# Optimization experiments

Measured on AMD Instinct MI355X. Metric: run time of the kernel, lower is better.

The kernel has to match this reference:

```python
import jax, jax.numpy as jnp
import numpy as np

D = 256       # d_model
H = 8         # nhead
W = 2048      # num windows (single drop level)
T = 64        # max_tokens per window (drop_info['num_sampled_tokens'][dl])
FILL = 48
N = W * FILL  # total voxels


def setup_inputs() -> dict:
    key = jax.random.key(0)
    k0, k1, k2, k3 = jax.random.split(key, 4)
    voxel_feat = jax.random.normal(k0, (N, D), jnp.float32)
    pos_embed = jax.random.normal(k1, (N, D), jnp.float32)
    # nn.MultiheadAttention params: packed in_proj [3D, D] and out_proj [D, D]
    in_proj_w = jax.random.normal(k2, (3 * D, D), jnp.float32) * (1.0 / np.sqrt(D))
    in_proj_b = jnp.zeros((3 * D,), jnp.float32)
    out_proj_w = jax.random.normal(k3, (D, D), jnp.float32) * (1.0 / np.sqrt(D))
    out_proj_b = jnp.zeros((D,), jnp.float32)
    # each voxel assigned a (window, in-window-slot) pair; slots unique per window
    window_idx = (jnp.arange(N) // FILL).astype(jnp.int32)
    slot_idx = (jnp.arange(N) % FILL).astype(jnp.int32)
    return {
        'voxel_feat': voxel_feat, 'pos_embed': pos_embed,
        'in_proj_w': in_proj_w, 'in_proj_b': in_proj_b,
        'out_proj_w': out_proj_w, 'out_proj_b': out_proj_b,
        'window_idx': window_idx, 'slot_idx': slot_idx,
        'num_windows': W, 'max_tokens': T,
    }


def reference(voxel_feat, pos_embed, in_proj_w, in_proj_b, out_proj_w, out_proj_b,
              window_idx, slot_idx, num_windows, max_tokens):
    Dm = voxel_feat.shape[-1]
    hd = Dm // H  # head dim
    P = num_windows * max_tokens  # padded token count
    valid = window_idx.astype(jnp.int32) * max_tokens + slot_idx.astype(jnp.int32)

    # scatter voxels into padded dense windows
    feat = jnp.zeros((P, Dm), voxel_feat.dtype).at[valid].set(voxel_feat)
    pos = jnp.ones((P, Dm), voxel_feat.dtype).at[valid].set(pos_embed)
    kmask = jnp.zeros((P,), bool).at[valid].set(True).reshape(num_windows, max_tokens)  # True = valid key
    feat = feat.reshape(num_windows, max_tokens, Dm)
    pos = pos.reshape(num_windows, max_tokens, Dm)

    # MHA: q = k = feat + pos, v = feat (torch nn.MultiheadAttention math)
    Wq, Wk, Wv = jnp.split(in_proj_w, 3, axis=0)
    bq, bk, bv = jnp.split(in_proj_b, 3, axis=0)
    qk_in = feat + pos
    q = (qk_in @ Wq.T + bq).reshape(num_windows, max_tokens, H, hd)
    k = (qk_in @ Wk.T + bk).reshape(num_windows, max_tokens, H, hd)
    v = (feat @ Wv.T + bv).reshape(num_windows, max_tokens, H, hd)

    scale = 1.0 / np.sqrt(hd)
    scores = jnp.einsum('wqhd,wkhd->whqk', q, k) * scale  # [W, H, T, T]
    scores = jnp.where(kmask[:, None, None, :], scores, -jnp.inf)  # key_padding_mask
    attn = jax.nn.softmax(scores, axis=-1)
    out = jnp.einsum('whqk,wkhd->wqhd', attn, v).reshape(P, Dm)
    out = out @ out_proj_w.T + out_proj_b

    # gather valid tokens back to per-voxel output (padded rows dropped, as in original)
    return out[valid]
```

## Files before the change

kernel.cpp:

```cpp
#include <hip/hip_runtime.h>

#define DD   256
#define HH   8
#define HDIM 32
#define TT   64
#define WW   2048

typedef unsigned short u16;
typedef __attribute__((ext_vector_type(8))) __bf16 bf8_t;
typedef __attribute__((ext_vector_type(4))) float  f32x4;

__device__ __forceinline__ u16 f2bf(float x) {
  union { float f; unsigned u; } c; c.f = x;
  unsigned r = c.u + 0x7FFFu + ((c.u >> 16) & 1u);
  return (u16)(r >> 16);
}
__device__ __forceinline__ int pack2(float a, float b) {
  return (int)((unsigned)f2bf(a) | ((unsigned)f2bf(b) << 16));
}

__global__ void prep_weights(const float* __restrict__ inw, const float* __restrict__ outw,
                             u16* __restrict__ wq, u16* __restrict__ wo) {
  int i = blockIdx.x * blockDim.x + threadIdx.x;
  if (i < 768 * 256) wq[i] = f2bf(inw[i]);
  if (i < 256 * 256) wo[i] = f2bf(outw[i]);
}

__global__ void build_slots(const int* __restrict__ widx, const int* __restrict__ sidx,
                            int* __restrict__ wslots, int n) {
  int i = blockIdx.x * blockDim.x + threadIdx.x;
  if (i < n) wslots[widx[i] * TT + sidx[i]] = i;
}

__global__ __launch_bounds__(512) void fused_attn(
    const float* __restrict__ feat, const float* __restrict__ pos,
    const u16* __restrict__ wqkv,
    const u16* __restrict__ wout,
    const float* __restrict__ inb, const float* __restrict__ outb,
    const int* __restrict__ wslots, float* __restrict__ out) {

  __shared__ int tl[TT];
  __shared__ u16 xqk[TT][72];
  __shared__ u16 xvs[TT][72];
  __shared__ u16 qld[TT][264];
  __shared__ u16 kld[TT][264];
  __shared__ u16 vtl[DD][72];

  const int t    = threadIdx.x;
  const int h    = t >> 6;
  const int lane = t & 63;
  const int g    = lane >> 4;
  const int l16  = lane & 15;
  const int w    = blockIdx.x;

  if (t < TT) tl[t] = wslots[w * TT + t];
  __syncthreads();

  const f32x4 zf = {0.f, 0.f, 0.f, 0.f};

  f32x4 qa[4][2], ka[4][2], va[2][4];
#pragma unroll
  for (int mt = 0; mt < 4; ++mt)
#pragma unroll
    for (int nt = 0; nt < 2; ++nt) { qa[mt][nt] = zf; ka[mt][nt] = zf; }
#pragma unroll
  for (int md = 0; md < 2; ++md)
#pragma unroll
    for (int nt = 0; nt < 4; ++nt) va[md][nt] = zf;

  const int stok = t >> 3;
  const int sds  = (t & 7) << 3;
  const int srow = tl[stok];

  for (int kc = 0; kc < 4; ++kc) {
    {
      union { u16 u[8]; bf8_t v; } aq, av_;
      if (srow >= 0) {
        const float4* fp = (const float4*)(feat + (size_t)srow * DD + kc * 64 + sds);
        const float4* pp = (const float4*)(pos  + (size_t)srow * DD + kc * 64 + sds);
        float4 f0 = fp[0], f1 = fp[1], p0 = pp[0], p1 = pp[1];
        float fr[8] = {f0.x, f0.y, f0.z, f0.w, f1.x, f1.y, f1.z, f1.w};
        float pr[8] = {p0.x, p0.y, p0.z, p0.w, p1.x, p1.y, p1.z, p1.w};
#pragma unroll
        for (int j = 0; j < 8; ++j) { aq.u[j] = f2bf(fr[j] + pr[j]); av_.u[j] = f2bf(fr[j]); }
      } else {
#pragma unroll
        for (int j = 0; j < 8; ++j) { aq.u[j] = 0; av_.u[j] = 0; }
      }
      *(bf8_t*)&xqk[stok][sds] = aq.v;
      *(bf8_t*)&xvs[stok][sds] = av_.v;
    }
    __syncthreads();

    bf8_t ax[4][2], bx[4][2];
#pragma unroll
    for (int mt = 0; mt < 4; ++mt)
#pragma unroll
      for (int ks = 0; ks < 2; ++ks) {
        ax[mt][ks] = *(const bf8_t*)&xqk[mt * 16 + l16][ks * 32 + g * 8];
        bx[mt][ks] = *(const bf8_t*)&xvs[mt * 16 + l16][ks * 32 + g * 8];
      }

#pragma unroll
    for (int ks = 0; ks < 2; ++ks) {
      const int kb = kc * 64 + ks * 32 + g * 8;
#pragma unroll
      for (int nt = 0; nt < 2; ++nt) {
        bf8_t bwq = *(const bf8_t*)(wqkv + (size_t)(h * 32 + nt * 16 + l16) * DD + kb);
#pragma unroll
        for (int mt = 0; mt < 4; ++mt)
          qa[mt][nt] = __builtin_amdgcn_mfma_f32_16x16x32_bf16(ax[mt][ks], bwq, qa[mt][nt], 0, 0, 0);
        bf8_t bwk = *(const bf8_t*)(wqkv + (size_t)(256 + h * 32 + nt * 16 + l16) * DD + kb);
#pragma unroll
        for (int mt = 0; mt < 4; ++mt)
          ka[mt][nt] = __builtin_amdgcn_mfma_f32_16x16x32_bf16(ax[mt][ks], bwk, ka[mt][nt], 0, 0, 0);
      }
#pragma unroll
      for (int md = 0; md < 2; ++md) {
        bf8_t awv = *(const bf8_t*)(wqkv + (size_t)(512 + h * 32 + md * 16 + l16) * DD + kb);
#pragma unroll
        for (int nt = 0; nt < 4; ++nt)
          va[md][nt] = __builtin_amdgcn_mfma_f32_16x16x32_bf16(awv, bx[nt][ks], va[md][nt], 0, 0, 0);
      }
    }
    __syncthreads();
  }

#pragma unroll
  for (int nt = 0; nt < 2; ++nt) {
    float bq = inb[h * 32 + nt * 16 + l16];
    float bk = inb[256 + h * 32 + nt * 16 + l16];
#pragma unroll
    for (int mt = 0; mt < 4; ++mt)
#pragma unroll
      for (int r = 0; r < 4; ++r) {
        qld[mt * 16 + 4 * g + r][h * 32 + nt * 16 + l16] = f2bf(qa[mt][nt][r] + bq);
        kld[mt * 16 + 4 * g + r][h * 32 + nt * 16 + l16] = f2bf(ka[mt][nt][r] + bk);
      }
  }
#pragma unroll
  for (int md = 0; md < 2; ++md)
#pragma unroll
    for (int r = 0; r < 4; ++r) {
      float bv = inb[512 + h * 32 + md * 16 + 4 * g + r];
#pragma unroll
      for (int nt = 0; nt < 4; ++nt)
        vtl[h * 32 + md * 16 + 4 * g + r][nt * 16 + l16] = f2bf(va[md][nt][r] + bv);
    }

  bf8_t akf[4], bqf[4];
#pragma unroll
  for (int mt = 0; mt < 4; ++mt) akf[mt] = *(const bf8_t*)&kld[mt * 16 + l16][h * 32 + g * 8];
#pragma unroll
  for (int nt = 0; nt < 4; ++nt) bqf[nt] = *(const bf8_t*)&qld[nt * 16 + l16][h * 32 + g * 8];

  f32x4 sa[4][4];
#pragma unroll
  for (int mt = 0; mt < 4; ++mt)
#pragma unroll
    for (int nt = 0; nt < 4; ++nt)
      sa[mt][nt] = __builtin_amdgcn_mfma_f32_16x16x32_bf16(akf[mt], bqf[nt], zf, 0, 0, 0);

  __syncthreads();

  bool vm[4][4];
#pragma unroll
  for (int mt = 0; mt < 4; ++mt)
#pragma unroll
    for (int r = 0; r < 4; ++r) vm[mt][r] = (tl[mt * 16 + 4 * g + r] >= 0);

  const float scale = 0.17677669529663687f;
  int pk[4][4][2];
#pragma unroll
  for (int nt = 0; nt < 4; ++nt) {
    float sv[4][4];
    float m = -3e38f;
#pragma unroll
    for (int mt = 0; mt < 4; ++mt)
#pragma unroll
      for (int r = 0; r < 4; ++r) {
        float s = vm[mt][r] ? sa[mt][nt][r] * scale : -3e38f;
        sv[mt][r] = s;
        m = fmaxf(m, s);
      }
    m = fmaxf(m, __shfl_xor(m, 16, 64));
    m = fmaxf(m, __shfl_xor(m, 32, 64));
    float sum = 0.f;
#pragma unroll
    for (int mt = 0; mt < 4; ++mt)
#pragma unroll
      for (int r = 0; r < 4; ++r) {
        float p = vm[mt][r] ? __expf(sv[mt][r] - m) : 0.f;
        sv[mt][r] = p;
        sum += p;
      }
    sum += __shfl_xor(sum, 16, 64);
    sum += __shfl_xor(sum, 32, 64);
    float inv = sum > 0.f ? 1.f / sum : 0.f;
#pragma unroll
    for (int mt = 0; mt < 4; ++mt)
#pragma unroll
      for (int rp = 0; rp < 2; ++rp)
        pk[mt][nt][rp] = pack2(sv[mt][2 * rp] * inv, sv[mt][2 * rp + 1] * inv);
  }

  bf8_t avf[2][2];
#pragma unroll
  for (int md = 0; md < 2; ++md)
#pragma unroll
    for (int kk = 0; kk < 2; ++kk)
      avf[md][kk] = *(const bf8_t*)&vtl[h * 32 + md * 16 + l16][kk * 32 + g * 8];

  f32x4 oa[2][4];
#pragma unroll
  for (int md = 0; md < 2; ++md)
#pragma unroll
    for (int nt = 0; nt < 4; ++nt) oa[md][nt] = zf;

#pragma unroll
  for (int kk = 0; kk < 2; ++kk) {
#pragma unroll
    for (int nt = 0; nt < 4; ++nt) {
      union { int wd[4]; bf8_t v; } bu;
#pragma unroll
      for (int wd = 0; wd < 4; ++wd) {
        int src = l16 + 16 * (2 * (g & 1) + (wd >> 1));
        int lo = __shfl(pk[2 * kk + 0][nt][wd & 1], src, 64);
        int hi = __shfl(pk[2 * kk + 1][nt][wd & 1], src, 64);
        bu.wd[wd] = (g & 2) ? hi : lo;
      }
#pragma unroll
      for (int md = 0; md < 2; ++md)
        oa[md][nt] = __builtin_amdgcn_mfma_f32_16x16x32_bf16(avf[md][kk], bu.v, oa[md][nt], 0, 0, 0);
    }
  }

#pragma unroll
  for (int md = 0; md < 2; ++md)
#pragma unroll
    for (int nt = 0; nt < 4; ++nt)
#pragma unroll
      for (int r = 0; r < 4; ++r)
        qld[nt * 16 + l16][h * 32 + md * 16 + 4 * g + r] = f2bf(oa[md][nt][r]);
  __syncthreads();

  f32x4 fa[4][2];
#pragma unroll
  for (int mt = 0; mt < 4; ++mt)
#pragma unroll
    for (int nt = 0; nt < 2; ++nt) fa[mt][nt] = zf;

#pragma unroll
  for (int kk = 0; kk < 8; ++kk) {
    bf8_t aa[4];
#pragma unroll
    for (int mt = 0; mt < 4; ++mt)
      aa[mt] = *(const bf8_t*)&qld[mt * 16 + l16][kk * 32 + g * 8];
#pragma unroll
    for (int nt = 0; nt < 2; ++nt) {
      bf8_t bw = *(const bf8_t*)(wout + (size_t)(h * 32 + nt * 16 + l16) * DD + kk * 32 + g * 8);
#pragma unroll
      for (int mt = 0; mt < 4; ++mt)
        fa[mt][nt] = __builtin_amdgcn_mfma_f32_16x16x32_bf16(aa[mt], bw, fa[mt][nt], 0, 0, 0);
    }
  }

#pragma unroll
  for (int nt = 0; nt < 2; ++nt) {
    float ob = outb[h * 32 + nt * 16 + l16];
#pragma unroll
    for (int mt = 0; mt < 4; ++mt)
#pragma unroll
      for (int r = 0; r < 4; ++r) {
        int tok = mt * 16 + 4 * g + r;
        int row = tl[tok];
        if (row >= 0)
          out[(size_t)row * DD + h * 32 + nt * 16 + l16] = fa[mt][nt][r] + ob;
      }
  }
}

extern "C" void kernel_launch(void* const* d_in, const int* in_sizes, int n_in,
                              void* d_out, int out_size, void* d_ws, size_t ws_size,
                              hipStream_t stream) {
  (void)n_in; (void)out_size; (void)ws_size;
  const float* feat = (const float*)d_in[0];
  const float* pos  = (const float*)d_in[1];
  const float* inw  = (const float*)d_in[2];
  const float* inb  = (const float*)d_in[3];
  const float* outw = (const float*)d_in[4];
  const float* outb = (const float*)d_in[5];
  const int*   widx = (const int*)d_in[6];
  const int*   sidx = (const int*)d_in[7];
  const int N = in_sizes[0] / DD;

  char* ws = (char*)d_ws;
  u16* wqkv   = (u16*)ws;
  u16* wout   = (u16*)(ws + 393216);
  int* wslots = (int*)(ws + 393216 + 131072);

  hipMemsetAsync(wslots, 0xFF, WW * TT * sizeof(int), stream);
  prep_weights<<<768, 256, 0, stream>>>(inw, outw, wqkv, wout);
  build_slots<<<(N + 255) / 256, 256, 0, stream>>>(widx, sidx, wslots, N);
  fused_attn<<<WW, 512, 0, stream>>>(feat, pos, wqkv, wout, inb, outb, wslots, (float*)d_out);
}
```

Before: 250.7 us.

## Alias shared buffers and split V and QK projections to cut LDS use

Shared memory is collapsed from five arrays into two aliased buffers. The whole feature row is now staged once, and the V projection runs before pos is added in place, followed by the Q/K projection. The aim is lower LDS use per block so more blocks fit per CU, plus fewer syncs inside the k-loop. The cost is extra barriers and an extra bf16 round-trip: q/k input becomes bf16(bf16(feat)+pos), which changes rounding slightly. The output store is also packed into an int2 write.

```diff
diff --git a/kernel.cpp b/kernel.cpp
--- a/kernel.cpp
+++ b/kernel.cpp
@@ -2,7 +2,6 @@
 
 #define DD   256
 #define HH   8
-#define HDIM 32
 #define TT   64
 #define WW   2048
 
@@ -14,6 +13,9 @@
   union { float f; unsigned u; } c; c.f = x;
   unsigned r = c.u + 0x7FFFu + ((c.u >> 16) & 1u);
   return (u16)(r >> 16);
+}
+__device__ __forceinline__ float bf2f(u16 x) {
+  union { unsigned u; float f; } c; c.u = ((unsigned)x) << 16; return c.f;
 }
 __device__ __forceinline__ int pack2(float a, float b) {
   return (int)((unsigned)f2bf(a) | ((unsigned)f2bf(b) << 16));
@@ -40,11 +42,8 @@
     const int* __restrict__ wslots, float* __restrict__ out) {
 
   __shared__ int tl[TT];
-  __shared__ u16 xqk[TT][72];
-  __shared__ u16 xvs[TT][72];
-  __shared__ u16 qld[TT][264];
-  __shared__ u16 kld[TT][264];
-  __shared__ u16 vtl[DD][72];
+  __shared__ u16 bufX[TT * 264];
+  __shared__ u16 bufY[DD * 72];
 
   const int t    = threadIdx.x;
   const int h    = t >> 6;
@@ -57,50 +56,89 @@
   __syncthreads();
 
   const f32x4 zf = {0.f, 0.f, 0.f, 0.f};
-
-  f32x4 qa[4][2], ka[4][2], va[2][4];
+  const int stok = t >> 3;
+  const int seg  = t & 7;
+  const int srow = tl[stok];
+
+  if (srow >= 0) {
+    const float4* fp = (const float4*)(feat + (size_t)srow * DD + seg * 32);
+    float4 f[8];
+#pragma unroll
+    for (int j = 0; j < 8; ++j) f[j] = fp[j];
+#pragma unroll
+    for (int c = 0; c < 4; ++c) {
+      union { u16 u[8]; bf8_t v; } r;
+#pragma unroll
+      for (int j = 0; j < 8; ++j) r.u[j] = f2bf(((const float*)f)[c * 8 + j]);
+      *(bf8_t*)&bufX[stok * 264 + seg * 32 + c * 8] = r.v;
+    }
+  } else {
+    union { u16 u[8]; bf8_t v; } z;
+#pragma unroll
+    for (int j = 0; j < 8; ++j) z.u[j] = 0;
+#pragma unroll
+    for (int c = 0; c < 4; ++c)
+      *(bf8_t*)&bufX[stok * 264 + seg * 32 + c * 8] = z.v;
+  }
+  __syncthreads();
+
+  f32x4 va[2][4];
+#pragma unroll
+  for (int md = 0; md < 2; ++md)
+#pragma unroll
+    for (int nt = 0; nt < 4; ++nt) va[md][nt] = zf;
+
+  for (int kc = 0; kc < 4; ++kc) {
+    bf8_t bx[4][2];
+#pragma unroll
+    for (int nt = 0; nt < 4; ++nt)
+#pragma unroll
+      for (int ks = 0; ks < 2; ++ks)
+        bx[nt][ks] = *(const bf8_t*)&bufX[(nt * 16 + l16) * 264 + kc * 64 + ks * 32 + g * 8];
+#pragma unroll
+    for (int ks = 0; ks < 2; ++ks) {
+      const int kb = kc * 64 + ks * 32 + g * 8;
+#pragma unroll
+      for (int md = 0; md < 2; ++md) {
+        bf8_t awv = *(const bf8_t*)(wqkv + (size_t)(512 + h * 32 + md * 16 + l16) * DD + kb);
+#pragma unroll
+        for (int nt = 0; nt < 4; ++nt)
+          va[md][nt] = __builtin_amdgcn_mfma_f32_16x16x32_bf16(awv, bx[nt][ks], va[md][nt], 0, 0, 0);
+      }
+    }
+  }
+  __syncthreads();
+
+  if (srow >= 0) {
+    const float4* pp = (const float4*)(pos + (size_t)srow * DD + seg * 32);
+    float4 p[8];
+#pragma unroll
+    for (int j = 0; j < 8; ++j) p[j] = pp[j];
+#pragma unroll
+    for (int c = 0; c < 4; ++c) {
+      union { u16 u[8]; bf8_t v; } xb, r;
+      xb.v = *(const bf8_t*)&bufX[stok * 264 + seg * 32 + c * 8];
+#pragma unroll
+      for (int j = 0; j < 8; ++j)
+        r.u[j] = f2bf(bf2f(xb.u[j]) + ((const float*)p)[c * 8 + j]);
+      *(bf8_t*)&bufX[stok * 264 + seg * 32 + c * 8] = r.v;
+    }
+  }
+  __syncthreads();
+
+  f32x4 qa[4][2], ka[4][2];
 #pragma unroll
   for (int mt = 0; mt < 4; ++mt)
 #pragma unroll
     for (int nt = 0; nt < 2; ++nt) { qa[mt][nt] = zf; ka[mt][nt] = zf; }
-#pragma unroll
-  for (int md = 0; md < 2; ++md)
-#pragma unroll
-    for (int nt = 0; nt < 4; ++nt) va[md][nt] = zf;
-
-  const int stok = t >> 3;
-  const int sds  = (t & 7) << 3;
-  const int srow = tl[stok];
 
   for (int kc = 0; kc < 4; ++kc) {
-    {
-      union { u16 u[8]; bf8_t v; } aq, av_;
-      if (srow >= 0) {
-        const float4* fp = (const float4*)(feat + (size_t)srow * DD + kc * 64 + sds);
-        const float4* pp = (const float4*)(pos  + (size_t)srow * DD + kc * 64 + sds);
-        float4 f0 = fp[0], f1 = fp[1], p0 = pp[0], p1 = pp[1];
-        float fr[8] = {f0.x, f0.y, f0.z, f0.w, f1.x, f1.y, f1.z, f1.w};
-        float pr[8] = {p0.x, p0.y, p0.z, p0.w, p1.x, p1.y, p1.z, p1.w};
-#pragma unroll
-        for (int j = 0; j < 8; ++j) { aq.u[j] = f2bf(fr[j] + pr[j]); av_.u[j] = f2bf(fr[j]); }
-      } else {
-#pragma unroll
-        for (int j = 0; j < 8; ++j) { aq.u[j] = 0; av_.u[j] = 0; }
-      }
-      *(bf8_t*)&xqk[stok][sds] = aq.v;
-      *(bf8_t*)&xvs[stok][sds] = av_.v;
-    }
-    __syncthreads();
-
-    bf8_t ax[4][2], bx[4][2];
-#pragma unroll
-    for (int mt = 0; mt < 4; ++mt)
-#pragma unroll
-      for (int ks = 0; ks < 2; ++ks) {
-        ax[mt][ks] = *(const bf8_t*)&xqk[mt * 16 + l16][ks * 32 + g * 8];
-        bx[mt][ks] = *(const bf8_t*)&xvs[mt * 16 + l16][ks * 32 + g * 8];
-      }
-
+    bf8_t ax[4][2];
+#pragma unroll
+    for (int mt = 0; mt < 4; ++mt)
+#pragma unroll
+      for (int ks = 0; ks < 2; ++ks)
+        ax[mt][ks] = *(const bf8_t*)&bufX[(mt * 16 + l16) * 264 + kc * 64 + ks * 32 + g * 8];
 #pragma unroll
     for (int ks = 0; ks < 2; ++ks) {
       const int kb = kc * 64 + ks * 32 + g * 8;
@@ -115,16 +153,9 @@
         for (int mt = 0; mt < 4; ++mt)
           ka[mt][nt] = __builtin_amdgcn_mfma_f32_16x16x32_bf16(ax[mt][ks], bwk, ka[mt][nt], 0, 0, 0);
       }
-#pragma unroll
-      for (int md = 0; md < 2; ++md) {
-        bf8_t awv = *(const bf8_t*)(wqkv + (size_t)(512 + h * 32 + md * 16 + l16) * DD + kb);
-#pragma unroll
-        for (int nt = 0; nt < 4; ++nt)
-          va[md][nt] = __builtin_amdgcn_mfma_f32_16x16x32_bf16(awv, bx[nt][ks], va[md][nt], 0, 0, 0);
-      }
-    }
-    __syncthreads();
-  }
+    }
+  }
+  __syncthreads();
 
 #pragma unroll
   for (int nt = 0; nt < 2; ++nt) {
@@ -134,10 +165,27 @@
     for (int mt = 0; mt < 4; ++mt)
 #pragma unroll
       for (int r = 0; r < 4; ++r) {
-        qld[mt * 16 + 4 * g + r][h * 32 + nt * 16 + l16] = f2bf(qa[mt][nt][r] + bq);
-        kld[mt * 16 + 4 * g + r][h * 32 + nt * 16 + l16] = f2bf(ka[mt][nt][r] + bk);
-      }
-  }
+        bufX[(mt * 16 + 4 * g + r) * 264 + h * 32 + nt * 16 + l16] = f2bf(qa[mt][nt][r] + bq);
+        bufY[(mt * 16 + 4 * g + r) * 264 + h * 32 + nt * 16 + l16] = f2bf(ka[mt][nt][r] + bk);
+      }
+  }
+  __syncthreads();
+
+  bf8_t akf[4], bqf[4];
+#pragma unroll
+  for (int mt = 0; mt < 4; ++mt) akf[mt] = *(const bf8_t*)&bufY[(mt * 16 + l16) * 264 + h * 32 + g * 8];
+#pragma unroll
+  for (int nt = 0; nt < 4; ++nt) bqf[nt] = *(const bf8_t*)&bufX[(nt * 16 + l16) * 264 + h * 32 + g * 8];
+
+  f32x4 sa[4][4];
+#pragma unroll
+  for (int mt = 0; mt < 4; ++mt)
+#pragma unroll
+    for (int nt = 0; nt < 4; ++nt)
+      sa[mt][nt] = __builtin_amdgcn_mfma_f32_16x16x32_bf16(akf[mt], bqf[nt], zf, 0, 0, 0);
+
+  __syncthreads();
+
 #pragma unroll
   for (int md = 0; md < 2; ++md)
 #pragma unroll
@@ -145,23 +193,8 @@
       float bv = inb[512 + h * 32 + md * 16 + 4 * g + r];
 #pragma unroll
       for (int nt = 0; nt < 4; ++nt)
-        vtl[h * 32 + md * 16 + 4 * g + r][nt * 16 + l16] = f2bf(va[md][nt][r] + bv);
-    }
-
-  bf8_t akf[4], bqf[4];
-#pragma unroll
-  for (int mt = 0; mt < 4; ++mt) akf[mt] = *(const bf8_t*)&kld[mt * 16 + l16][h * 32 + g * 8];
-#pragma unroll
-  for (int nt = 0; nt < 4; ++nt) bqf[nt] = *(const bf8_t*)&qld[nt * 16 + l16][h * 32 + g * 8];
-
-  f32x4 sa[4][4];
-#pragma unroll
-  for (int mt = 0; mt < 4; ++mt)
-#pragma unroll
-    for (int nt = 0; nt < 4; ++nt)
-      sa[mt][nt] = __builtin_amdgcn_mfma_f32_16x16x32_bf16(akf[mt], bqf[nt], zf, 0, 0, 0);
-
-  __syncthreads();
+        bufY[(h * 32 + md * 16 + 4 * g + r) * 72 + nt * 16 + l16] = f2bf(va[md][nt][r] + bv);
+    }
 
   bool vm[4][4];
 #pragma unroll
@@ -209,7 +242,7 @@
   for (int md = 0; md < 2; ++md)
 #pragma unroll
     for (int kk = 0; kk < 2; ++kk)
-      avf[md][kk] = *(const bf8_t*)&vtl[h * 32 + md * 16 + l16][kk * 32 + g * 8];
+      avf[md][kk] = *(const bf8_t*)&bufY[(h * 32 + md * 16 + l16) * 72 + kk * 32 + g * 8];
 
   f32x4 oa[2][4];
 #pragma unroll
@@ -238,10 +271,12 @@
 #pragma unroll
   for (int md = 0; md < 2; ++md)
 #pragma unroll
-    for (int nt = 0; nt < 4; ++nt)
-#pragma unroll
-      for (int r = 0; r < 4; ++r)
-        qld[nt * 16 + l16][h * 32 + md * 16 + 4 * g + r] = f2bf(oa[md][nt][r]);
+    for (int nt = 0; nt < 4; ++nt) {
+      union { int wd[2]; } pw;
+      pw.wd[0] = pack2(oa[md][nt][0], oa[md][nt][1]);
+      pw.wd[1] = pack2(oa[md][nt][2], oa[md][nt][3]);
+      *(int2*)&bufX[(nt * 16 + l16) * 264 + h * 32 + md * 16 + 4 * g] = make_int2(pw.wd[0], pw.wd[1]);
+    }
   __syncthreads();
 
   f32x4 fa[4][2];
@@ -255,7 +290,7 @@
     bf8_t aa[4];
 #pragma unroll
     for (int mt = 0; mt < 4; ++mt)
-      aa[mt] = *(const bf8_t*)&qld[mt * 16 + l16][kk * 32 + g * 8];
+      aa[mt] = *(const bf8_t*)&bufX[(mt * 16 + l16) * 264 + kk * 32 + g * 8];
 #pragma unroll
     for (int nt = 0; nt < 2; ++nt) {
       bf8_t bw = *(const bf8_t*)(wout + (size_t)(h * 32 + nt * 16 + l16) * DD + kk * 32 + g * 8);
```

New measurement: 255.7 us. 1.02x slower.

## Split fused window attention into a dense QKV GEMM kernel and an attention/out-proj kernel

Applied to the files above, without the earlier changes.

Replaces the single per-window fused kernel with two kernels. The first projects Q, K and V with a dense GEMM over the voxels, so padded tokens are not computed, and writes Q/K in bf16 plus V transposed per window. The second computes attention and the output projection with 256-thread blocks, two heads per wave, and a swizzled LDS layout. The aim is to cut wasted MFMA work on padding and to improve occupancy, at the cost of extra global round-trips for the Q/K/V intermediates and a scattered transposed V write. It also assumes N is a multiple of 64 and that unused V slots are never read unmasked (they can be uninitialized).

```diff
diff --git a/kernel.cpp b/kernel.cpp
--- a/kernel.cpp
+++ b/kernel.cpp
@@ -1,14 +1,14 @@
 #include <hip/hip_runtime.h>
 
-#define DD   256
-#define HH   8
-#define HDIM 32
-#define TT   64
-#define WW   2048
+#define DD 256
+#define TT 64
+#define WW 2048
 
 typedef unsigned short u16;
 typedef __attribute__((ext_vector_type(8))) __bf16 bf8_t;
 typedef __attribute__((ext_vector_type(4))) float  f32x4;
+
+#define XSW(tok, col) ((tok) * 256 + ((col) ^ (((tok) & 7) << 3)))
 
 __device__ __forceinline__ u16 f2bf(float x) {
   union { float f; unsigned u; } c; c.f = x;
@@ -32,22 +32,144 @@
   if (i < n) wslots[widx[i] * TT + sidx[i]] = i;
 }
 
-__global__ __launch_bounds__(512) void fused_attn(
+__global__ __launch_bounds__(256, 4) void qkv_gemm(
     const float* __restrict__ feat, const float* __restrict__ pos,
-    const u16* __restrict__ wqkv,
-    const u16* __restrict__ wout,
-    const float* __restrict__ inb, const float* __restrict__ outb,
+    const u16* __restrict__ wqkv, const float* __restrict__ inb,
+    const int* __restrict__ widx, const int* __restrict__ sidx,
+    u16* __restrict__ qc, u16* __restrict__ kc, u16* __restrict__ vt) {
+
+  __shared__ u16 xb[TT * 72];
+  __shared__ u16 cb[TT * 264];
+
+  const int t    = threadIdx.x;
+  const int wv   = t >> 6;
+  const int lane = t & 63;
+  const int g    = lane >> 4;
+  const int l16  = lane & 15;
+  const int m0   = blockIdx.x * 64;
+  const int p    = blockIdx.y;
+
+  const int svox = t >> 2;
+  const int sseg = t & 3;
+
+  const f32x4 zf = {0.f, 0.f, 0.f, 0.f};
+  f32x4 acc[4][4];
+#pragma unroll
+  for (int mt = 0; mt < 4; ++mt)
+#pragma unroll
+    for (int nt = 0; nt < 4; ++nt) acc[mt][nt] = zf;
+
+  for (int kc_ = 0; kc_ < 4; ++kc_) {
+    {
+      const float4* fp = (const float4*)(feat + (size_t)(m0 + svox) * DD + kc_ * 64 + sseg * 16);
+      float4 f[4];
+#pragma unroll
+      for (int j = 0; j < 4; ++j) f[j] = fp[j];
+      float fr[16];
+#pragma unroll
+      for (int j = 0; j < 16; ++j) fr[j] = ((const float*)f)[j];
+      if (p < 2) {
+        const float4* pp = (const float4*)(pos + (size_t)(m0 + svox) * DD + kc_ * 64 + sseg * 16);
+        float4 q[4];
+#pragma unroll
+        for (int j = 0; j < 4; ++j) q[j] = pp[j];
+#pragma unroll
+        for (int j = 0; j < 16; ++j) fr[j] += ((const float*)q)[j];
+      }
+#pragma unroll
+      for (int c = 0; c < 2; ++c) {
+        union { u16 u[8]; bf8_t v; } r;
+#pragma unroll
+        for (int j = 0; j < 8; ++j) r.u[j] = f2bf(fr[c * 8 + j]);
+        *(bf8_t*)&xb[svox * 72 + sseg * 16 + c * 8] = r.v;
+      }
+    }
+    __syncthreads();
+
+    if (p < 2) {
+      bf8_t ax[4][2];
+#pragma unroll
+      for (int mt = 0; mt < 4; ++mt)
+#pragma unroll
+        for (int ks = 0; ks < 2; ++ks)
+          ax[mt][ks] = *(const bf8_t*)&xb[(mt * 16 + l16) * 72 + ks * 32 + g * 8];
+#pragma unroll
+      for (int ks = 0; ks < 2; ++ks) {
+        const int kb = kc_ * 64 + ks * 32 + g * 8;
+#pragma unroll
+        for (int nt = 0; nt < 4; ++nt) {
+          bf8_t bw = *(const bf8_t*)(wqkv + (size_t)(p * 256 + wv * 64 + nt * 16 + l16) * DD + kb);
+#pragma unroll
+          for (int mt = 0; mt < 4; ++mt)
+            acc[mt][nt] = __builtin_amdgcn_mfma_f32_16x16x32_bf16(ax[mt][ks], bw, acc[mt][nt], 0, 0, 0);
+        }
+      }
+    } else {
+      bf8_t bx[4][2];
+#pragma unroll
+      for (int nt = 0; nt < 4; ++nt)
+#pragma unroll
+        for (int ks = 0; ks < 2; ++ks)
+          bx[nt][ks] = *(const bf8_t*)&xb[(nt * 16 + l16) * 72 + ks * 32 + g * 8];
+#pragma unroll
+      for (int ks = 0; ks < 2; ++ks) {
+        const int kb = kc_ * 64 + ks * 32 + g * 8;
+#pragma unroll
+        for (int mt = 0; mt < 4; ++mt) {
+          bf8_t aw = *(const bf8_t*)(wqkv + (size_t)(512 + wv * 64 + mt * 16 + l16) * DD + kb);
+#pragma unroll
+          for (int nt = 0; nt < 4; ++nt)
+            acc[mt][nt] = __builtin_amdgcn_mfma_f32_16x16x32_bf16(aw, bx[nt][ks], acc[mt][nt], 0, 0, 0);
+        }
+      }
+    }
+    __syncthreads();
+  }
+
+  if (p < 2) {
+#pragma unroll
+    for (int nt = 0; nt < 4; ++nt) {
+      float b = inb[p * 256 + wv * 64 + nt * 16 + l16];
+#pragma unroll
+      for (int mt = 0; mt < 4; ++mt)
+#pragma unroll
+        for (int r = 0; r < 4; ++r)
+          cb[(mt * 16 + 4 * g + r) * 264 + wv * 64 + nt * 16 + l16] = f2bf(acc[mt][nt][r] + b);
+    }
+    __syncthreads();
+    u16* dst = p ? kc : qc;
+#pragma unroll
+    for (int it = 0; it < 8; ++it) {
+      int i = it * 256 + t;
+      int row = i >> 5, c8 = (i & 31) * 8;
+      *(bf8_t*)&dst[(size_t)(m0 + row) * DD + c8] = *(const bf8_t*)&cb[row * 264 + c8];
+    }
+  } else {
+#pragma unroll
+    for (int nt = 0; nt < 4; ++nt) {
+      int vx = m0 + nt * 16 + l16;
+      size_t bw_ = (size_t)widx[vx] * (DD * TT) + sidx[vx];
+#pragma unroll
+      for (int mt = 0; mt < 4; ++mt)
+#pragma unroll
+        for (int r = 0; r < 4; ++r) {
+          int vd = wv * 64 + mt * 16 + 4 * g + r;
+          vt[bw_ + (size_t)vd * TT] = f2bf(acc[mt][nt][r] + inb[512 + vd]);
+        }
+    }
+  }
+}
+
+__global__ __launch_bounds__(256, 4) void attn_out(
+    const u16* __restrict__ qc, const u16* __restrict__ kc, const u16* __restrict__ vt,
+    const u16* __restrict__ wout, const float* __restrict__ outb,
     const int* __restrict__ wslots, float* __restrict__ out) {
 
   __shared__ int tl[TT];
-  __shared__ u16 xqk[TT][72];
-  __shared__ u16 xvs[TT][72];
-  __shared__ u16 qld[TT][264];
-  __shared__ u16 kld[TT][264];
-  __shared__ u16 vtl[DD][72];
+  __shared__ u16 ab[TT * 256];
 
   const int t    = threadIdx.x;
-  const int h    = t >> 6;
+  const int wv   = t >> 6;
   const int lane = t & 63;
   const int g    = lane >> 4;
   const int l16  = lane & 15;
@@ -58,207 +180,128 @@
 
   const f32x4 zf = {0.f, 0.f, 0.f, 0.f};
 
-  f32x4 qa[4][2], ka[4][2], va[2][4];
+  bool vm[4][4];
 #pragma unroll
   for (int mt = 0; mt < 4; ++mt)
 #pragma unroll
-    for (int nt = 0; nt < 2; ++nt) { qa[mt][nt] = zf; ka[mt][nt] = zf; }
-#pragma unroll
-  for (int md = 0; md < 2; ++md)
-#pragma unroll
-    for (int nt = 0; nt < 4; ++nt) va[md][nt] = zf;
-
-  const int stok = t >> 3;
-  const int sds  = (t & 7) << 3;
-  const int srow = tl[stok];
-
-  for (int kc = 0; kc < 4; ++kc) {
-    {
-      union { u16 u[8]; bf8_t v; } aq, av_;
-      if (srow >= 0) {
-        const float4* fp = (const float4*)(feat + (size_t)srow * DD + kc * 64 + sds);
-        const float4* pp = (const float4*)(pos  + (size_t)srow * DD + kc * 64 + sds);
-        float4 f0 = fp[0], f1 = fp[1], p0 = pp[0], p1 = pp[1];
-        float fr[8] = {f0.x, f0.y, f0.z, f0.w, f1.x, f1.y, f1.z, f1.w};
-        float pr[8] = {p0.x, p0.y, p0.z, p0.w, p1.x, p1.y, p1.z, p1.w};
-#pragma unroll
-        for (int j = 0; j < 8; ++j) { aq.u[j] = f2bf(fr[j] + pr[j]); av_.u[j] = f2bf(fr[j]); }
-      } else {
-#pragma unroll
-        for (int j = 0; j < 8; ++j) { aq.u[j] = 0; av_.u[j] = 0; }
-      }
-      *(bf8_t*)&xqk[stok][sds] = aq.v;
-      *(bf8_t*)&xvs[stok][sds] = av_.v;
-    }
-    __syncthreads();
-
-    bf8_t ax[4][2], bx[4][2];
+    for (int r = 0; r < 4; ++r) vm[mt][r] = (tl[mt * 16 + 4 * g + r] >= 0);
+
+#pragma unroll 1
+  for (int hh = 0; hh < 2; ++hh) {
+    const int h = wv * 2 + hh;
+
+    bf8_t akf[4], bqf[4];
+#pragma unroll
+    for (int mt = 0; mt < 4; ++mt) {
+      int row = tl[mt * 16 + l16]; row = row < 0 ? 0 : row;
+      akf[mt] = *(const bf8_t*)&kc[(size_t)row * DD + h * 32 + g * 8];
+    }
+#pragma unroll
+    for (int nt = 0; nt < 4; ++nt) {
+      int row = tl[nt * 16 + l16]; row = row < 0 ? 0 : row;
+      bqf[nt] = *(const bf8_t*)&qc[(size_t)row * DD + h * 32 + g * 8];
+    }
+
+    f32x4 sa[4][4];
 #pragma unroll
     for (int mt = 0; mt < 4; ++mt)
 #pragma unroll
-      for (int ks = 0; ks < 2; ++ks) {
-        ax[mt][ks] = *(const bf8_t*)&xqk[mt * 16 + l16][ks * 32 + g * 8];
-        bx[mt][ks] = *(const bf8_t*)&xvs[mt * 16 + l16][ks * 32 + g * 8];
-      }
-
-#pragma unroll
-    for (int ks = 0; ks < 2; ++ks) {
-      const int kb = kc * 64 + ks * 32 + g * 8;
-#pragma unroll
-      for (int nt = 0; nt < 2; ++nt) {
-        bf8_t bwq = *(const bf8_t*)(wqkv + (size_t)(h * 32 + nt * 16 + l16) * DD + kb);
-#pragma unroll
-        for (int mt = 0; mt < 4; ++mt)
-          qa[mt][nt] = __builtin_amdgcn_mfma_f32_16x16x32_bf16(ax[mt][ks], bwq, qa[mt][nt], 0, 0, 0);
-        bf8_t bwk = *(const bf8_t*)(wqkv + (size_t)(256 + h * 32 + nt * 16 + l16) * DD + kb);
-#pragma unroll
-        for (int mt = 0; mt < 4; ++mt)
-          ka[mt][nt] = __builtin_amdgcn_mfma_f32_16x16x32_bf16(ax[mt][ks], bwk, ka[mt][nt], 0, 0, 0);
-      }
-#pragma unroll
-      for (int md = 0; md < 2; ++md) {
-        bf8_t awv = *(const bf8_t*)(wqkv + (size_t)(512 + h * 32 + md * 16 + l16) * DD + kb);
-#pragma unroll
-        for (int nt = 0; nt < 4; ++nt)
-          va[md][nt] = __builtin_amdgcn_mfma_f32_16x16x32_bf16(awv, bx[nt][ks], va[md][nt], 0, 0, 0);
-      }
-    }
-    __syncthreads();
-  }
-
-#pragma unroll
-  for (int nt = 0; nt < 2; ++nt) {
-    float bq = inb[h * 32 + nt * 16 + l16];
-    float bk = inb[256 + h * 32 + nt * 16 + l16];
-#pragma unroll
-    for (int mt = 0; mt < 4; ++mt)
-#pragma unroll
-      for (int r = 0; r < 4; ++r) {
-        qld[mt * 16 + 4 * g + r][h * 32 + nt * 16 + l16] = f2bf(qa[mt][nt][r] + bq);
-        kld[mt * 16 + 4 * g + r][h * 32 + nt * 16 + l16] = f2bf(ka[mt][nt][r] + bk);
-      }
-  }
-#pragma unroll
-  for (int md = 0; md < 2; ++md)
-#pragma unroll
-    for (int r = 0; r < 4; ++r) {
-      float bv = inb[512 + h * 32 + md * 16 + 4 * g + r];
-#pragma unroll
       for (int nt = 0; nt < 4; ++nt)
-        vtl[h * 32 + md * 16 + 4 * g + r][nt * 16 + l16] = f2bf(va[md][nt][r] + bv);
-    }
-
-  bf8_t akf[4], bqf[4];
-#pragma unroll
-  for (int mt = 0; mt < 4; ++mt) akf[mt] = *(const bf8_t*)&kld[mt * 16 + l16][h * 32 + g * 8];
-#pragma unroll
-  for (int nt = 0; nt < 4; ++nt) bqf[nt] = *(const bf8_t*)&qld[nt * 16 + l16][h * 32 + g * 8];
-
-  f32x4 sa[4][4];
+        sa[mt][nt] = __builtin_amdgcn_mfma_f32_16x16x32_bf16(akf[mt], bqf[nt], zf, 0, 0, 0);
+
+    const float scale = 0.17677669529663687f;
+    int pk[4][4][2];
+#pragma unroll
+    for (int nt = 0; nt < 4; ++nt) {
+      float sv[4][4];
+      float m = -3e38f;
+#pragma unroll
+      for (int mt = 0; mt < 4; ++mt)
+#pragma unroll
+        for (int r = 0; r < 4; ++r) {
+          float s = vm[mt][r] ? sa[mt][nt][r] * scale : -3e38f;
+          sv[mt][r] = s;
+          m = fmaxf(m, s);
+        }
+      m = fmaxf(m, __shfl_xor(m, 16, 64));
+      m = fmaxf(m, __shfl_xor(m, 32, 64));
+      float sum = 0.f;
+#pragma unroll
+      for (int mt = 0; mt < 4; ++mt)
+#pragma unroll
+        for (int r = 0; r < 4; ++r) {
+          float pv = vm[mt][r] ? __expf(sv[mt][r] - m) : 0.f;
+          sv[mt][r] = pv;
+          sum += pv;
+        }
+      sum += __shfl_xor(sum, 16, 64);
+      sum += __shfl_xor(sum, 32, 64);
+      float inv = sum > 0.f ? 1.f / sum : 0.f;
+#pragma unroll
+      for (int mt = 0; mt < 4; ++mt)
+#pragma unroll
+        for (int rp = 0; rp < 2; ++rp)
+          pk[mt][nt][rp] = pack2(sv[mt][2 * rp] * inv, sv[mt][2 * rp + 1] * inv);
+    }
+
+    bf8_t avf[2][2];
+#pragma unroll
+    for (int md = 0; md < 2; ++md)
+#pragma unroll
+      for (int kk = 0; kk < 2; ++kk)
+        avf[md][kk] = *(const bf8_t*)&vt[(size_t)w * (DD * TT) +
+                                        (size_t)(h * 32 + md * 16 + l16) * TT + kk * 32 + g * 8];
+
+    f32x4 oa[2][4];
+#pragma unroll
+    for (int md = 0; md < 2; ++md)
+#pragma unroll
+      for (int nt = 0; nt < 4; ++nt) oa[md][nt] = zf;
+
+#pragma unroll
+    for (int kk = 0; kk < 2; ++kk) {
+#pragma unroll
+      for (int nt = 0; nt < 4; ++nt) {
+        union { int wd[4]; bf8_t v; } bu;
+#pragma unroll
+        for (int wd = 0; wd < 4; ++wd) {
+          int src = l16 + 16 * (2 * (g & 1) + (wd >> 1));
+          int lo = __shfl(pk[2 * kk + 0][nt][wd & 1], src, 64);
+          int hi = __shfl(pk[2 * kk + 1][nt][wd & 1], src, 64);
+          bu.wd[wd] = (g & 2) ? hi : lo;
+        }
+#pragma unroll
+        for (int md = 0; md < 2; ++md)
+          oa[md][nt] = __builtin_amdgcn_mfma_f32_16x16x32_bf16(avf[md][kk], bu.v, oa[md][nt], 0, 0, 0);
+      }
+    }
+
+#pragma unroll
+    for (int md = 0; md < 2; ++md)
+#pragma unroll
+      for (int nt = 0; nt < 4; ++nt) {
+        int w0 = pack2(oa[md][nt][0], oa[md][nt][1]);
+        int w1 = pack2(oa[md][nt][2], oa[md][nt][3]);
+        *(int2*)&ab[XSW(nt * 16 + l16, h * 32 + md * 16 + 4 * g)] = make_int2(w0, w1);
+      }
+  }
+  __syncthreads();
+
+  f32x4 fa[4][4];
 #pragma unroll
   for (int mt = 0; mt < 4; ++mt)
 #pragma unroll
-    for (int nt = 0; nt < 4; ++nt)
-      sa[mt][nt] = __builtin_amdgcn_mfma_f32_16x16x32_bf16(akf[mt], bqf[nt], zf, 0, 0, 0);
-
-  __syncthreads();
-
-  bool vm[4][4];
-#pragma unroll
-  for (int mt = 0; mt < 4; ++mt)
-#pragma unroll
-    for (int r = 0; r < 4; ++r) vm[mt][r] = (tl[mt * 16 + 4 * g + r] >= 0);
-
-  const float scale = 0.17677669529663687f;
-  int pk[4][4][2];
-#pragma unroll
-  for (int nt = 0; nt < 4; ++nt) {
-    float sv[4][4];
-    float m = -3e38f;
-#pragma unroll
-    for (int mt = 0; mt < 4; ++mt)
-#pragma unroll
-      for (int r = 0; r < 4; ++r) {
-        float s = vm[mt][r] ? sa[mt][nt][r] * scale : -3e38f;
-        sv[mt][r] = s;
-        m = fmaxf(m, s);
-      }
-    m = fmaxf(m, __shfl_xor(m, 16, 64));
-    m = fmaxf(m, __shfl_xor(m, 32, 64));
-    float sum = 0.f;
-#pragma unroll
-    for (int mt = 0; mt < 4; ++mt)
-#pragma unroll
-      for (int r = 0; r < 4; ++r) {
-        float p = vm[mt][r] ? __expf(sv[mt][r] - m) : 0.f;
-        sv[mt][r] = p;
-        sum += p;
-      }
-    sum += __shfl_xor(sum, 16, 64);
-    sum += __shfl_xor(sum, 32, 64);
-    float inv = sum > 0.f ? 1.f / sum : 0.f;
-#pragma unroll
-    for (int mt = 0; mt < 4; ++mt)
-#pragma unroll
-      for (int rp = 0; rp < 2; ++rp)
-        pk[mt][nt][rp] = pack2(sv[mt][2 * rp] * inv, sv[mt][2 * rp + 1] * inv);
-  }
-
-  bf8_t avf[2][2];
-#pragma unroll
-  for (int md = 0; md < 2; ++md)
-#pragma unroll
-    for (int kk = 0; kk < 2; ++kk)
-      avf[md][kk] = *(const bf8_t*)&vtl[h * 32 + md * 16 + l16][kk * 32 + g * 8];
-
-  f32x4 oa[2][4];
-#pragma unroll
-  for (int md = 0; md < 2; ++md)
-#pragma unroll
-    for (int nt = 0; nt < 4; ++nt) oa[md][nt] = zf;
-
-#pragma unroll
-  for (int kk = 0; kk < 2; ++kk) {
-#pragma unroll
-    for (int nt = 0; nt < 4; ++nt) {
-      union { int wd[4]; bf8_t v; } bu;
-#pragma unroll
-      for (int wd = 0; wd < 4; ++wd) {
-        int src = l16 + 16 * (2 * (g & 1) + (wd >> 1));
-        int lo = __shfl(pk[2 * kk + 0][nt][wd & 1], src, 64);
-        int hi = __shfl(pk[2 * kk + 1][nt][wd & 1], src, 64);
-        bu.wd[wd] = (g & 2) ? hi : lo;
-      }
-#pragma unroll
-      for (int md = 0; md < 2; ++md)
-        oa[md][nt] = __builtin_amdgcn_mfma_f32_16x16x32_bf16(avf[md][kk], bu.v, oa[md][nt], 0, 0, 0);
-    }
-  }
-
-#pragma unroll
-  for (int md = 0; md < 2; ++md)
-#pragma unroll
-    for (int nt = 0; nt < 4; ++nt)
-#pragma unroll
-      for (int r = 0; r < 4; ++r)
-        qld[nt * 16 + l16][h * 32 + md * 16 + 4 * g + r] = f2bf(oa[md][nt][r]);
-  __syncthreads();
-
-  f32x4 fa[4][2];
-#pragma unroll
-  for (int mt = 0; mt < 4; ++mt)
-#pragma unroll
-    for (int nt = 0; nt < 2; ++nt) fa[mt][nt] = zf;
+    for (int nt = 0; nt < 4; ++nt) fa[mt][nt] = zf;
 
 #pragma unroll
   for (int kk = 0; kk < 8; ++kk) {
     bf8_t aa[4];
 #pragma unroll
     for (int mt = 0; mt < 4; ++mt)
-      aa[mt] = *(const bf8_t*)&qld[mt * 16 + l16][kk * 32 + g * 8];
-#pragma unroll
-    for (int nt = 0; nt < 2; ++nt) {
-      bf8_t bw = *(const bf8_t*)(wout + (size_t)(h * 32 + nt * 16 + l16) * DD + kk * 32 + g * 8);
+      aa[mt] = *(const bf8_t*)&ab[XSW(mt * 16 + l16, kk * 32 + g * 8)];
+#pragma unroll
+    for (int nt = 0; nt < 4; ++nt) {
+      bf8_t bw = *(const bf8_t*)(wout + (size_t)(wv * 64 + nt * 16 + l16) * DD + kk * 32 + g * 8);
 #pragma unroll
       for (int mt = 0; mt < 4; ++mt)
         fa[mt][nt] = __builtin_amdgcn_mfma_f32_16x16x32_bf16(aa[mt], bw, fa[mt][nt], 0, 0, 0);
@@ -266,16 +309,15 @@
   }
 
 #pragma unroll
-  for (int nt = 0; nt < 2; ++nt) {
-    float ob = outb[h * 32 + nt * 16 + l16];
+  for (int nt = 0; nt < 4; ++nt) {
+    float ob = outb[wv * 64 + nt * 16 + l16];
 #pragma unroll
     for (int mt = 0; mt < 4; ++mt)
 #pragma unroll
       for (int r = 0; r < 4; ++r) {
-        int tok = mt * 16 + 4 * g + r;
-        int row = tl[tok];
+        int row = tl[mt * 16 + 4 * g + r];
         if (row >= 0)
-          out[(size_t)row * DD + h * 32 + nt * 16 + l16] = fa[mt][nt][r] + ob;
+          out[(size_t)row * DD + wv * 64 + nt * 16 + l16] = fa[mt][nt][r] + ob;
       }
   }
 }
@@ -298,9 +340,14 @@
   u16* wqkv   = (u16*)ws;
   u16* wout   = (u16*)(ws + 393216);
   int* wslots = (int*)(ws + 393216 + 131072);
+  size_t off  = 1048576;
+  u16* qc = (u16*)(ws + off); off += (size_t)N * DD * 2;
+  u16* kc = (u16*)(ws + off); off += (size_t)N * DD * 2;
+  u16* vt = (u16*)(ws + off);
 
   hipMemsetAsync(wslots, 0xFF, WW * TT * sizeof(int), stream);
   prep_weights<<<768, 256, 0, stream>>>(inw, outw, wqkv, wout);
   build_slots<<<(N + 255) / 256, 256, 0, stream>>>(widx, sidx, wslots, N);
-  fused_attn<<<WW, 512, 0, stream>>>(feat, pos, wqkv, wout, inb, outb, wslots, (float*)d_out);
-}
+  qkv_gemm<<<dim3(N / 64, 3), 256, 0, stream>>>(feat, pos, wqkv, inb, widx, sidx, qc, kc, vt);
+  attn_out<<<WW, 256, 0, stream>>>(qc, kc, vt, wout, outb, wslots, (float*)d_out);
+}
```

After: 351.5 us. 1.4x slower.
